# Optimization experiments

Hardware: AMD Instinct MI355X
Metric: run time of the kernel (lower is better)

The kernel has to match this reference:

```python
import jax, jax.numpy as jnp
import numpy as np

D_MODEL = 2048
D_INNER = 4096      # expand * d_model
HEADDIM = 64
NHEADS = 64         # d_inner // headdim
D_STATE = 128
NGROUPS = 1
D_CONV = 4
CHUNK = 128
EPS = 1e-5
BATCH = 2
SEQLEN = 4096
D_CONV_CH = D_INNER + 2 * NGROUPS * D_STATE            # 4352
D_IN_PROJ = 2 * D_INNER + 2 * NGROUPS * D_STATE + NHEADS  # 8512


def setup_inputs() -> dict:
    ks = jax.random.split(jax.random.key(0), 9)
    u = jax.random.normal(ks[0], (BATCH, SEQLEN, D_MODEL), jnp.float32)
    W_in = jax.random.normal(ks[1], (D_MODEL, D_IN_PROJ), jnp.float32) * 0.02
    conv_w = jax.random.normal(ks[2], (D_CONV_CH, D_CONV), jnp.float32) * 0.2
    conv_b = jax.random.normal(ks[3], (D_CONV_CH,), jnp.float32) * 0.02
    dt_bias = jax.random.normal(ks[4], (NHEADS,), jnp.float32) * 0.1
    A_log = jax.random.normal(ks[5], (NHEADS,), jnp.float32) * 0.1
    D = jnp.ones((NHEADS,), jnp.float32)
    norm_w = jnp.ones((D_INNER,), jnp.float32)
    W_out = jax.random.normal(ks[8], (D_INNER, D_MODEL), jnp.float32) * 0.02
    return dict(u=u, W_in=W_in, conv_w=conv_w, conv_b=conv_b, dt_bias=dt_bias,
                A_log=A_log, D=D, norm_w=norm_w, W_out=W_out)


def _mamba2_forward(u, W_in, conv_w, conv_b, dt_bias, A_log, D, norm_w, W_out):
    b, L, _ = u.shape
    zxbcdt = u @ W_in                                       # (b, L, 8512)
    z = zxbcdt[..., :D_INNER]
    xBC = zxbcdt[..., D_INNER:D_INNER + D_CONV_CH]
    dt = zxbcdt[..., D_INNER + D_CONV_CH:]                  # (b, L, h)

    # causal depthwise conv1d (padding = d_conv-1, truncated to L) + SiLU
    padded = jnp.pad(xBC, ((0, 0), (D_CONV - 1, 0), (0, 0)))
    xBC_conv = conv_b + sum(padded[:, k:k + L, :] * conv_w[:, k] for k in range(D_CONV))
    xBC_act = jax.nn.silu(xBC_conv)

    x = xBC_act[..., :D_INNER].reshape(b, L, NHEADS, HEADDIM)
    Bm = xBC_act[..., D_INNER:D_INNER + NGROUPS * D_STATE].reshape(b, L, NGROUPS, D_STATE)
    Cm = xBC_act[..., D_INNER + NGROUPS * D_STATE:].reshape(b, L, NGROUPS, D_STATE)
    rep = NHEADS // NGROUPS
    Bh = jnp.repeat(Bm, rep, axis=2)                        # (b, L, h, n)
    Ch = jnp.repeat(Cm, rep, axis=2)

    A = -jnp.exp(A_log)                                     # (h,), negative
    dtf = jax.nn.softplus(dt + dt_bias)                     # (b, L, h)

    # ---- chunked SSD (structured state-space duality) scan ----
    nc = L // CHUNK
    xc = x.reshape(b, nc, CHUNK, NHEADS, HEADDIM)
    Bc = Bh.reshape(b, nc, CHUNK, NHEADS, D_STATE)
    Cc = Ch.reshape(b, nc, CHUNK, NHEADS, D_STATE)
    dtc = dtf.reshape(b, nc, CHUNK, NHEADS)
    cum = jnp.cumsum(dtc * A, axis=2)                       # (b, nc, cs, h), decreasing

    # intra-chunk causal decay matrix L_ij = exp(cum_i - cum_j), i >= j
    idx = jnp.arange(CHUNK)
    mask = (idx[:, None] >= idx[None, :])[None, None, :, :, None]
    seg = cum[:, :, :, None, :] - cum[:, :, None, :, :]     # (b, nc, i, j, h)
    decay = jnp.exp(jnp.where(mask, seg, -jnp.inf))
    CB = jnp.einsum('bcihn,bcjhn->bcijh', Cc, Bc)
    Y_diag = jnp.einsum('bcijh,bcjh,bcjhp->bcihp', CB * decay, dtc, xc)

    # per-chunk final states: sum_j exp(cum_last - cum_j) * dt_j * B_j (x) x_j
    decay_last = jnp.exp(cum[:, :, -1:, :] - cum)           # (b, nc, cs, h)
    states = jnp.einsum('bclh,bclhn,bclhp->bchpn', decay_last * dtc, Bc, xc)

    # inter-chunk recurrence: carry_{c+1} = exp(sum dA_c) * carry_c + states_c
    Atot = jnp.exp(cum[:, :, -1, :])                        # (b, nc, h)
    def step(carry, inp):
        a, s = inp
        return a[..., None, None] * carry + s, carry
    init = jnp.zeros((b, NHEADS, HEADDIM, D_STATE), jnp.float32)
    _, prev = jax.lax.scan(step, init, (jnp.moveaxis(Atot, 1, 0), jnp.moveaxis(states, 1, 0)))
    prev = jnp.moveaxis(prev, 0, 1)                         # (b, nc, h, p, n) state entering each chunk

    Y_off = jnp.einsum('bclhn,bclh,bchpn->bclhp', Cc, jnp.exp(cum), prev)

    y = (Y_diag + Y_off).reshape(b, L, NHEADS, HEADDIM) + D[:, None] * x
    y = y.reshape(b, L, D_INNER)

    # gated RMSNorm: rmsnorm(y * silu(z)) * norm_w
    t = y * jax.nn.silu(z)
    t = t * jax.lax.rsqrt(jnp.mean(t * t, axis=-1, keepdims=True) + EPS) * norm_w
    return t @ W_out


def reference(u, W_in, conv_w, conv_b, dt_bias, A_log, D, norm_w, W_out):
    return _mamba2_forward(u, W_in, conv_w, conv_b, dt_bias, A_log, D, norm_w, W_out)
```

## Files before the change

### kernel.cpp

```cpp
#include <hip/hip_runtime.h>

#define BATCH 2
#define SEQLEN 4096
#define DM 2048
#define DIP 8512
#define DIPP 8576
#define DI 4096
#define DCC 4352
#define NH 64
#define HD 64
#define DSZ 128
#define CHK 128
#define NC 32
#define NBL (BATCH*SEQLEN)
#define LDP 136

typedef __attribute__((ext_vector_type(4))) float f32x4;
typedef __attribute__((ext_vector_type(8))) __bf16 bf16x8;
typedef __attribute__((ext_vector_type(8))) unsigned short us8;
typedef __attribute__((ext_vector_type(4))) unsigned short us4;

__device__ inline float bf2f(unsigned short u){ union{unsigned int i; float f;} v; v.i=((unsigned)u)<<16; return v.f; }
__device__ inline unsigned short f2bf(float f){ union{float f; unsigned int i;} v; v.f=f; unsigned r=(v.i + 0x7FFFu + ((v.i>>16)&1u))>>16; return (unsigned short)r; }

#define GLOAD_LDS16(gp, lp) __builtin_amdgcn_global_load_lds( \
    (const __attribute__((address_space(1))) void*)(gp), \
    (__attribute__((address_space(3))) void*)(lp), 16, 0, 0)

__global__ void beacon_kernel(float* __restrict__ out, float v)
{
    if (blockIdx.x == 0 && threadIdx.x == 0) out[0] = v;
}

__global__ void cast_bf16_kernel(const float* __restrict__ src, unsigned short* __restrict__ dst, size_t n)
{
    size_t stride = (size_t)gridDim.x * blockDim.x * 8;
    for (size_t i = ((size_t)blockIdx.x*blockDim.x + threadIdx.x)*8; i < n; i += stride) {
        float4 a = *(const float4*)&src[i];
        float4 b = *(const float4*)&src[i+4];
        us8 o;
        o[0]=f2bf(a.x); o[1]=f2bf(a.y); o[2]=f2bf(a.z); o[3]=f2bf(a.w);
        o[4]=f2bf(b.x); o[5]=f2bf(b.y); o[6]=f2bf(b.z); o[7]=f2bf(b.w);
        *(us8*)&dst[i] = o;
    }
}

__global__ __launch_bounds__(256) void transpose_cast_kernel(
    const float* __restrict__ in, unsigned short* __restrict__ out, int R, int C)
{
    __shared__ float tile[32][33];
    const int c0 = blockIdx.x*32, r0 = blockIdx.y*32;
    const int tx = threadIdx.x & 31, ty = threadIdx.x >> 5;
    #pragma unroll
    for (int i = 0; i < 4; i++) {
        const int r = r0 + ty + i*8;
        const int c = c0 + tx;
        tile[ty+i*8][tx] = (c < C) ? in[(size_t)r*C + c] : 0.f;
    }
    __syncthreads();
    #pragma unroll
    for (int i = 0; i < 4; i++) {
        const int cc = c0 + ty + i*8;
        const int rr = r0 + tx;
        out[(size_t)cc*R + rr] = f2bf(tile[tx][ty+i*8]);
    }
}

template<int EPI>
__global__ __launch_bounds__(512, 2) void gemm256(
    const unsigned short* __restrict__ A, const unsigned short* __restrict__ Bt,
    float* __restrict__ C, int K, int ldc, int Nmax,
    unsigned short* __restrict__ zbf, unsigned short* __restrict__ xbcbf,
    float* __restrict__ dtf, const float* __restrict__ dt_bias)
{
    __shared__ unsigned short L[65536];
    const int m0 = blockIdx.x * 256;
    const int n0 = blockIdx.y * 256;
    const int tid = threadIdx.x;
    const int lane = tid & 63;
    const int wid  = tid >> 6;
    const int wm = wid >> 2, wn = wid & 3;
    const int lr  = lane & 15;
    const int lkg = (lane >> 4) * 8;
    const int srow = (wid << 4) + (lane >> 3);
    const int scol = ((lane & 7) ^ (lane >> 3)) << 3;
    const int cs0 = lkg ^ ((lr & 7) << 3);
    const int cs1 = cs0 ^ 32;
    const int nt = K >> 6;

    f32x4 acc[8][4];
    #pragma unroll
    for (int i=0;i<8;i++)
        #pragma unroll
        for (int j=0;j<4;j++) acc[i][j] = f32x4{0.f,0.f,0.f,0.f};

    auto stA = [&](int buf, int t, int h) {
        const unsigned short* g = A + (size_t)(m0 + h*128 + srow)*K + t*64 + scol;
        GLOAD_LDS16(g,               &L[buf*32768 + h*8192 + wid*1024]);
        GLOAD_LDS16(g + (size_t)8*K, &L[buf*32768 + h*8192 + wid*1024 + 512]);
    };
    auto stB = [&](int buf, int t, int h) {
        const int rr = n0 + h*128 + srow;
        const int r0 = (rr     > Nmax) ? Nmax : rr;
        const int r1 = (rr + 8 > Nmax) ? Nmax : rr + 8;
        GLOAD_LDS16(Bt + (size_t)r0*K + t*64 + scol, &L[buf*32768 + 16384 + h*8192 + wid*1024]);
        GLOAD_LDS16(Bt + (size_t)r1*K + t*64 + scol, &L[buf*32768 + 16384 + h*8192 + wid*1024 + 512]);
    };

    bf16x8 bfr[4][2];
    auto rdA = [&](int buf, int mq, int s, int ks) {
        const int rl = mq*32 + s*16 + lr;
        return *(const bf16x8*)&L[buf*32768 + wm*8192 + rl*64 + (ks ? cs1 : cs0)];
    };
    auto rdB = [&](int buf, int nf, int ks) {
        const int rl = (wn & 1)*64 + nf*16 + lr;
        return *(const bf16x8*)&L[buf*32768 + 16384 + (wn >> 1)*8192 + rl*64 + (ks ? cs1 : cs0)];
    };

#define PH(BUF, MQ, LOADB, ...) do { \
    bf16x8 af[2][2]; \
    af[0][0]=rdA(BUF,MQ,0,0); af[0][1]=rdA(BUF,MQ,0,1); \
    af[1][0]=rdA(BUF,MQ,1,0); af[1][1]=rdA(BUF,MQ,1,1); \
    if (LOADB) { \
        _Pragma("unroll") \
        for (int nf=0;nf<4;nf++){ bfr[nf][0]=rdB(BUF,nf,0); bfr[nf][1]=rdB(BUF,nf,1);} } \
    __VA_ARGS__; \
    asm volatile("s_barrier" ::: "memory"); \
    __builtin_amdgcn_s_setprio(1); \
    _Pragma("unroll") \
    for (int s=0;s<2;s++) { \
        _Pragma("unroll") \
        for (int nf=0;nf<4;nf++) { \
            acc[MQ*2+s][nf] = __builtin_amdgcn_mfma_f32_16x16x32_bf16(af[s][0], bfr[nf][0], acc[MQ*2+s][nf], 0,0,0); \
            acc[MQ*2+s][nf] = __builtin_amdgcn_mfma_f32_16x16x32_bf16(af[s][1], bfr[nf][1], acc[MQ*2+s][nf], 0,0,0); } } \
    __builtin_amdgcn_s_setprio(0); \
    asm volatile("s_barrier" ::: "memory"); \
} while(0)

    stA(0, 0, 0); stA(0, 0, 1); stB(0, 0, 0); stB(0, 0, 1);
    stB(1, 1, 0); stB(1, 1, 1);
    asm volatile("s_waitcnt vmcnt(4)" ::: "memory");
    asm volatile("s_barrier" ::: "memory");

    #pragma unroll 1
    for (int t = 0; t < nt; t += 2) {
        const int tp2 = (t + 2 < nt) ? t + 2 : nt - 1;
        const int tp3 = (t + 3 < nt) ? t + 3 : nt - 1;
        PH(0, 0, true,  stA(1, t+1, 0));
        PH(0, 1, false, stA(1, t+1, 1); stB(0, tp2, 0));
        PH(0, 2, false, stB(0, tp2, 1));
        PH(0, 3, false, asm volatile("s_waitcnt vmcnt(4)" ::: "memory"));
        PH(1, 0, true,  stA(0, tp2, 0));
        PH(1, 1, false, stA(0, tp2, 1); stB(1, tp3, 0));
        PH(1, 2, false, stB(1, tp3, 1));
        PH(1, 3, false, asm volatile("s_waitcnt vmcnt(4)" ::: "memory"));
    }
#undef PH

    const int cr = (lane >> 4) * 4;
    const int cc = lane & 15;
    #pragma unroll
    for (int i=0;i<8;i++) {
        #pragma unroll
        for (int j=0;j<4;j++) {
            const int row = m0 + wm*128 + i*16 + cr;
            const int col = n0 + wn*64 + j*16 + cc;
            #pragma unroll
            for (int r=0;r<4;r++) {
                const float val = acc[i][j][r];
                const int rr = row + r;
                if (EPI == 0) {
                    C[(size_t)rr*ldc + col] = val;
                } else {
                    if (col < DI) {
                        zbf[(size_t)rr*DI + col] = f2bf(val);
                    } else if (col < DI + DCC) {
                        xbcbf[(size_t)rr*DCC + (col - DI)] = f2bf(val);
                    } else if (col < DI + DCC + NH) {
                        const int hh = col - (DI + DCC);
                        const float x = val + dt_bias[hh];
                        dtf[(size_t)rr*NH + hh] = (x > 20.f) ? x : log1pf(__expf(x));
                    }
                }
            }
        }
    }
}

__global__ __launch_bounds__(256) void conv_x_kernel(
    const unsigned short* __restrict__ xbc,
    const float* __restrict__ cw, const float* __restrict__ cb,
    unsigned short* __restrict__ xT)
{
    __shared__ float raw[67][68];
    __shared__ unsigned short ot[64][72];
    const int lt = blockIdx.x;
    const int h  = blockIdx.y;
    const int b  = lt >> 6;
    const int l0 = (lt & 63) * 64;
    const int t = threadIdx.x;

    for (int i = t; i < 536; i += 256) {
        const int li = i >> 3, cg = (i & 7) * 8;
        const int l = l0 - 3 + li;
        us8 v;
        #pragma unroll
        for (int e = 0; e < 8; e++) v[e] = 0;
        if (l >= 0) v = *(const us8*)&xbc[(size_t)(b*SEQLEN + l)*DCC + h*64 + cg];
        #pragma unroll
        for (int e = 0; e < 8; e++) raw[li][cg+e] = bf2f(v[e]);
    }
    __syncthreads();
    #pragma unroll
    for (int j = 0; j < 16; j++) {
        const int i = t + j*256;
        const int l = i >> 6, p = i & 63;
        const int ch = h*64 + p;
        float a = cb[ch];
        #pragma unroll
        for (int k = 0; k < 4; k++) a += raw[l + k][p] * cw[ch*4 + k];
        a = a / (1.f + __expf(-a));
        ot[l][p] = f2bf(a);
    }
    __syncthreads();
    for (int i = t; i < 512; i += 256) {
        const int p = i >> 3, lg = (i & 7) * 8;
        us8 o;
        #pragma unroll
        for (int e = 0; e < 8; e++) o[e] = ot[lg + e][p];
        *(us8*)&xT[(size_t)((b*NH + h)*HD + p)*SEQLEN + l0 + lg] = o;
    }
}

__global__ void conv_bc_kernel(const unsigned short* __restrict__ xbc,
                               const float* __restrict__ cw, const float* __restrict__ cb,
                               unsigned short* __restrict__ bcbf)
{
    const int idx = blockIdx.x*256 + threadIdx.x;
    if (idx >= NBL*32) return;
    const int g = idx & 31;
    const int row = idx >> 5;
    const int l = row & (SEQLEN-1);
    const int ch0 = DI + g*8;
    float a[8];
    #pragma unroll
    for (int e=0;e<8;e++) a[e] = cb[ch0+e];
    #pragma unroll
    for (int k = 0; k < 4; k++) {
        if (l + k >= 3) {
            us8 v = *(const us8*)&xbc[(size_t)(row + k - 3)*DCC + ch0];
            #pragma unroll
            for (int e=0;e<8;e++) a[e] += bf2f(v[e]) * cw[(ch0+e)*4 + k];
        }
    }
    us8 o;
    #pragma unroll
    for (int e=0;e<8;e++){ const float s = a[e]/(1.f+__expf(-a[e])); o[e]=f2bf(s); }
    *(us8*)&bcbf[(size_t)row*256 + g*8] = o;
}

__global__ void cum_kernel(const float* __restrict__ dtf, const float* __restrict__ A_log,
                           float* __restrict__ cum)
{
    const int idx = blockIdx.x*256 + threadIdx.x;
    const int h = idx & 63;
    const int bc = idx >> 6;
    const float A = -__expf(A_log[h]);
    float c = 0.f;
    const float* src = dtf + (size_t)bc*CHK*NH + h;
    float* dst = cum + (size_t)bc*CHK*NH + h;
    for (int i = 0; i < CHK; i++) { c += src[i*NH]*A; dst[i*NH] = c; }
}

__global__ __launch_bounds__(256) void ssm_passS(
    const unsigned short* __restrict__ bcbf,
    const unsigned short* __restrict__ xT,
    const float* __restrict__ cumg,
    const float* __restrict__ dtfg,
    unsigned short* __restrict__ states)
{
    __shared__ unsigned short BT[128*LDP];
    __shared__ unsigned short XW[64*LDP];
    __shared__ float cum_s[128], dtc_s[128], w_s[128];

    const int blk = blockIdx.x;
    const int h = blk & 63;
    const int bc = blk >> 6;
    const int r0 = bc * CHK;
    const int t = threadIdx.x;
    const int lane = t & 63;
    const int wid = t >> 6;

    if (t < 128) {
        cum_s[t] = cumg[(size_t)(r0+t)*NH + h];
        dtc_s[t] = dtfg[(size_t)(r0+t)*NH + h];
    }
    for (int i = t; i < 2048; i += 256) {
        const int l = i >> 4, cg = (i & 15)*8;
        us8 v = *(const us8*)(bcbf + (size_t)(r0+l)*256 + cg);
        #pragma unroll
        for (int e = 0; e < 8; e++) BT[(cg+e)*LDP + l] = v[e];
    }
    __syncthreads();
    if (t < 128) w_s[t] = __expf(cum_s[127] - cum_s[t]) * dtc_s[t];
    __syncthreads();
    {
        const int b = bc >> 5;
        const int li = (bc & 31) * CHK;
        const unsigned short* xb = xT + (size_t)((b*NH + h)*HD)*SEQLEN + li;
        for (int i = t; i < 1024; i += 256) {
            const int p = i >> 4, cg = (i & 15)*8;
            us8 v = *(const us8*)(xb + (size_t)p*SEQLEN + cg);
            #pragma unroll
            for (int e = 0; e < 8; e++) v[e] = f2bf(bf2f(v[e]) * w_s[cg+e]);
            *(us8*)&XW[p*LDP + cg] = v;
        }
    }
    __syncthreads();

    const int lr = lane & 15;
    const int lkg = (lane >> 4)*8;
    const int wr = wid >> 1, wc = wid & 1;

    f32x4 acc[2][4];
    #pragma unroll
    for (int i=0;i<2;i++)
        #pragma unroll
        for (int j=0;j<4;j++) acc[i][j] = f32x4{0.f,0.f,0.f,0.f};
    #pragma unroll
    for (int k = 0; k < 4; k++) {
        bf16x8 a[2], b[4];
        #pragma unroll
        for (int i=0;i<2;i++) a[i] = *(const bf16x8*)&XW[(wr*32 + i*16 + lr)*LDP + k*32 + lkg];
        #pragma unroll
        for (int j=0;j<4;j++) b[j] = *(const bf16x8*)&BT[(wc*64 + j*16 + lr)*LDP + k*32 + lkg];
        #pragma unroll
        for (int i=0;i<2;i++)
            #pragma unroll
            for (int j=0;j<4;j++)
                acc[i][j] = __builtin_amdgcn_mfma_f32_16x16x32_bf16(a[i], b[j], acc[i][j], 0,0,0);
    }
    unsigned short* sb = states + (size_t)blk * (HD*DSZ);
    const int cr = (lane >> 4)*4, cc = lane & 15;
    #pragma unroll
    for (int i=0;i<2;i++) {
        #pragma unroll
        for (int j=0;j<4;j++) {
            const int nn = wc*64 + j*16 + cc;
            #pragma unroll
            for (int r=0;r<4;r++) {
                const int pp = wr*32 + i*16 + cr + r;
                sb[pp*DSZ + nn] = f2bf(acc[i][j][r]);
            }
        }
    }
}

__global__ void scan_kernel(unsigned short* __restrict__ states, const float* __restrict__ cumg)
{
    const int idx = blockIdx.x*256 + threadIdx.x;
    const int n = idx & 127;
    const int p = (idx >> 7) & 63;
    const int h = (idx >> 13) & 63;
    const int b = idx >> 19;
    float carry = 0.f;
    for (int c = 0; c < NC; c++) {
        const size_t off = ((size_t)((b*NC + c)*NH + h))*(HD*DSZ) + p*DSZ + n;
        const float s = bf2f(states[off]);
        states[off] = f2bf(carry);
        const float atot = __expf(cumg[(size_t)((b*NC+c)*CHK + 127)*NH + h]);
        carry = atot*carry + s;
    }
}

__global__ __launch_bounds__(256) void ssm_passY(
    const unsigned short* __restrict__ bcbf,
    const unsigned short* __restrict__ xT,
    const unsigned short* __restrict__ statesg,
    const float* __restrict__ cumg,
    const float* __restrict__ dtfg,
    const float* __restrict__ Dg,
    unsigned short* __restrict__ y)
{
    __shared__ unsigned short P1[128*LDP];
    __shared__ unsigned short P2[128*LDP];
    __shared__ unsigned short XTs[64*LDP];
    __shared__ unsigned short PV[64*LDP];
    __shared__ float cum_s[128], dtc_s[128];

    const int blk = blockIdx.x;
    const int h = blk & 63;
    const int bc = blk >> 6;
    const int r0 = bc * CHK;
    const int t = threadIdx.x;
    const int lane = t & 63;
    const int wid = t >> 6;

    if (t < 128) {
        cum_s[t] = cumg[(size_t)(r0+t)*NH + h];
        dtc_s[t] = dtfg[(size_t)(r0+t)*NH + h];
    }
    for (int i = t; i < 2048; i += 256) {
        const int l = i >> 4, cg = (i & 15)*8;
        const unsigned short* src = bcbf + (size_t)(r0+l)*256 + cg;
        *(us8*)&P2[l*LDP + cg] = *(const us8*)src;
        *(us8*)&P1[l*LDP + cg] = *(const us8*)(src + 128);
    }
    {
        const int b = bc >> 5;
        const int li = (bc & 31) * CHK;
        const unsigned short* xb = xT + (size_t)((b*NH + h)*HD)*SEQLEN + li;
        const unsigned short* sb = statesg + (size_t)blk * (HD*DSZ);
        for (int i = t; i < 1024; i += 256) {
            const int p = i >> 4, cg = (i & 15)*8;
            *(us8*)&XTs[p*LDP + cg] = *(const us8*)(xb + (size_t)p*SEQLEN + cg);
            *(us8*)&PV[p*LDP + cg]  = *(const us8*)(sb + p*DSZ + cg);
        }
    }
    __syncthreads();

    const int lr = lane & 15;
    const int lkg = (lane >> 4)*8;
    const int wr = wid >> 1, wc = wid & 1;

    f32x4 acc1[4][4], acc2[4][2];
    #pragma unroll
    for (int i=0;i<4;i++) {
        #pragma unroll
        for (int j=0;j<4;j++) acc1[i][j] = f32x4{0.f,0.f,0.f,0.f};
        #pragma unroll
        for (int j=0;j<2;j++) acc2[i][j] = f32x4{0.f,0.f,0.f,0.f};
    }
    #pragma unroll
    for (int k = 0; k < 4; k++) {
        bf16x8 a[4], b[4], pv[2];
        #pragma unroll
        for (int i=0;i<4;i++) a[i] = *(const bf16x8*)&P1[(wr*64 + i*16 + lr)*LDP + k*32 + lkg];
        #pragma unroll
        for (int j=0;j<4;j++) b[j] = *(const bf16x8*)&P2[(wc*64 + j*16 + lr)*LDP + k*32 + lkg];
        #pragma unroll
        for (int j=0;j<2;j++) pv[j] = *(const bf16x8*)&PV[(wc*32 + j*16 + lr)*LDP + k*32 + lkg];
        #pragma unroll
        for (int i=0;i<4;i++) {
            #pragma unroll
            for (int j=0;j<4;j++)
                acc1[i][j] = __builtin_amdgcn_mfma_f32_16x16x32_bf16(a[i], b[j], acc1[i][j], 0,0,0);
            #pragma unroll
            for (int j=0;j<2;j++)
                acc2[i][j] = __builtin_amdgcn_mfma_f32_16x16x32_bf16(a[i], pv[j], acc2[i][j], 0,0,0);
        }
    }
    __syncthreads();
    const int cr = (lane >> 4)*4, cc = lane & 15;
    #pragma unroll
    for (int i=0;i<4;i++) {
        #pragma unroll
        for (int j=0;j<4;j++) {
            const int jj = wc*64 + j*16 + cc;
            #pragma unroll
            for (int r=0;r<4;r++) {
                const int ii = wr*64 + i*16 + cr + r;
                float v = 0.f;
                if (jj <= ii) v = acc1[i][j][r] * __expf(cum_s[ii] - cum_s[jj]) * dtc_s[jj];
                P1[ii*LDP + jj] = f2bf(v);
            }
        }
    }
    __syncthreads();
    #pragma unroll
    for (int i=0;i<4;i++) {
        #pragma unroll
        for (int r=0;r<4;r++) {
            const int ii = wr*64 + i*16 + cr + r;
            const float sc = __expf(cum_s[ii]);
            #pragma unroll
            for (int j=0;j<2;j++) acc2[i][j][r] *= sc;
        }
    }
    #pragma unroll
    for (int k = 0; k < 4; k++) {
        bf16x8 a[4], x2[2];
        #pragma unroll
        for (int i=0;i<4;i++) a[i] = *(const bf16x8*)&P1[(wr*64 + i*16 + lr)*LDP + k*32 + lkg];
        #pragma unroll
        for (int j=0;j<2;j++) x2[j] = *(const bf16x8*)&XTs[(wc*32 + j*16 + lr)*LDP + k*32 + lkg];
        #pragma unroll
        for (int i=0;i<4;i++)
            #pragma unroll
            for (int j=0;j<2;j++)
                acc2[i][j] = __builtin_amdgcn_mfma_f32_16x16x32_bf16(a[i], x2[j], acc2[i][j], 0,0,0);
    }
    const float Dv = Dg[h];
    #pragma unroll
    for (int i=0;i<4;i++) {
        #pragma unroll
        for (int j=0;j<2;j++) {
            const int pp = wc*32 + j*16 + cc;
            #pragma unroll
            for (int r=0;r<4;r++) {
                const int ii = wr*64 + i*16 + cr + r;
                const float xv = bf2f(XTs[pp*LDP + ii]);
                y[(size_t)(r0+ii)*DI + h*64 + pp] = f2bf(acc2[i][j][r] + Dv * xv);
            }
        }
    }
}

__global__ __launch_bounds__(256) void gate_rms_kernel(
    const unsigned short* __restrict__ y, const unsigned short* __restrict__ z,
    const float* __restrict__ nw, unsigned short* __restrict__ tbf)
{
    const int row = blockIdx.x;
    const int t = threadIdx.x;
    const int lane = t & 63, wid = t >> 6;
    float tv[16];
    float ss = 0.f;
    #pragma unroll
    for (int i = 0; i < 2; i++) {
        const int c = (i*256 + t)*8;
        const us8 yv = *(const us8*)&y[(size_t)row*DI + c];
        const us8 zv = *(const us8*)&z[(size_t)row*DI + c];
        #pragma unroll
        for (int e = 0; e < 8; e++) {
            const float fy = bf2f(yv[e]);
            const float fz = bf2f(zv[e]);
            const float v = fy * (fz / (1.f + __expf(-fz)));
            tv[i*8+e] = v;
            ss += v*v;
        }
    }
    #pragma unroll
    for (int o = 1; o < 64; o <<= 1) ss += __shfl_xor(ss, o, 64);
    __shared__ float red[4];
    if (lane == 0) red[wid] = ss;
    __syncthreads();
    const float rms = rsqrtf((red[0]+red[1]+red[2]+red[3]) * (1.f/DI) + 1e-5f);
    #pragma unroll
    for (int i = 0; i < 2; i++) {
        const int c = (i*256 + t)*8;
        us8 o;
        #pragma unroll
        for (int e = 0; e < 8; e += 4) {
            const float4 wv = *(const float4*)&nw[c + e];
            o[e+0]=f2bf(tv[i*8+e+0]*rms*wv.x);
            o[e+1]=f2bf(tv[i*8+e+1]*rms*wv.y);
            o[e+2]=f2bf(tv[i*8+e+2]*rms*wv.z);
            o[e+3]=f2bf(tv[i*8+e+3]*rms*wv.w);
        }
        *(us8*)&tbf[(size_t)row*DI + c] = o;
    }
}

extern "C" void kernel_launch(void* const* d_in, const int* in_sizes, int n_in,
                              void* d_out, int out_size, void* d_ws, size_t ws_size,
                              hipStream_t stream)
{
    const float* u       = (const float*)d_in[0];
    const float* W_in    = (const float*)d_in[1];
    const float* conv_w  = (const float*)d_in[2];
    const float* conv_b  = (const float*)d_in[3];
    const float* dt_bias = (const float*)d_in[4];
    const float* A_log   = (const float*)d_in[5];
    const float* Dp      = (const float*)d_in[6];
    const float* norm_w  = (const float*)d_in[7];
    const float* W_out   = (const float*)d_in[8];
    float* out = (float*)d_out;

    char* ws = (char*)d_ws;
    const size_t OFF_WINT = 33554432;
    const size_t OFF_R2   = 68681728;
    const size_t OFF_R3   = 139984896;
    const size_t OFF_SM   = 207093760;
    const size_t NEED     = OFF_SM + 2097152 + 2097152 + 4194304;
    if (ws_size < NEED) {
        beacon_kernel<<<1, 64, 0, stream>>>(out, 10000.f + (float)(ws_size >> 20));
        return;
    }

    unsigned short* u_bf   = (unsigned short*)(ws);
    unsigned short* winT   = (unsigned short*)(ws + OFF_WINT);
    unsigned short* xTb    = (unsigned short*)(ws);
    unsigned short* t_bf   = (unsigned short*)(ws);
    unsigned short* xbc_bf = (unsigned short*)(ws + OFF_R2);
    unsigned short* y_bf   = (unsigned short*)(ws + OFF_R2);
    unsigned short* states = (unsigned short*)(ws + OFF_R3);
    unsigned short* woutT  = (unsigned short*)(ws + OFF_R3);
    float*          dtf    = (float*)(ws + OFF_SM);
    float*          cum    = (float*)(ws + OFF_SM + 2097152);
    unsigned short* bc_bf  = (unsigned short*)(ws + OFF_SM + 4194304);
    unsigned short* z_bf   = (unsigned short*)d_out;

    cast_bf16_kernel<<<2048, 256, 0, stream>>>(u, u_bf, (size_t)NBL*DM);
    transpose_cast_kernel<<<dim3(DIPP/32, DM/32), 256, 0, stream>>>(W_in, winT, DM, DIP);
    gemm256<1><<<dim3(NBL/256, (DIPP+255)/256), 512, 0, stream>>>(
        u_bf, winT, nullptr, DM, 0, DIPP-1, z_bf, xbc_bf, dtf, dt_bias);
    conv_x_kernel<<<dim3(NBL/64, NH), 256, 0, stream>>>(xbc_bf, conv_w, conv_b, xTb);
    conv_bc_kernel<<<(NBL*32)/256, 256, 0, stream>>>(xbc_bf, conv_w, conv_b, bc_bf);
    cum_kernel<<<16, 256, 0, stream>>>(dtf, A_log, cum);
    ssm_passS<<<BATCH*NC*NH, 256, 0, stream>>>(bc_bf, xTb, cum, dtf, states);
    scan_kernel<<<4096, 256, 0, stream>>>(states, cum);
    ssm_passY<<<BATCH*NC*NH, 256, 0, stream>>>(bc_bf, xTb, states, cum, dtf, Dp, y_bf);
    gate_rms_kernel<<<NBL, 256, 0, stream>>>(y_bf, z_bf, norm_w, t_bf);
    transpose_cast_kernel<<<dim3(DM/32, DI/32), 256, 0, stream>>>(W_out, woutT, DI, DM);
    gemm256<0><<<dim3(NBL/256, DM/256), 512, 0, stream>>>(
        t_bf, woutT, out, DI, DM, DM-1, nullptr, nullptr, nullptr, nullptr);
}
```

Baseline: 958.2 us.

## Fuse BC conv into conv_x, read SSM operands directly from global, tweak GEMM bounds

Folds the B/C depthwise convolution into conv_x_kernel as four extra block rows, removing one kernel launch. ssm_passS and ssm_passY drop most of their shared-memory staging and feed MFMA fragments straight from global memory, which cuts LDS use and allows three blocks per CU, at the cost of uncoalesced, latency-exposed global loads inside the MFMA loop. The GEMM launch bounds change from two blocks per CU to one, which gives the compiler more registers but lowers occupancy, and an lgkmcnt wait is added before the barrier. cum_kernel now launches 64 blocks of 64 threads.

```diff
diff --git a/kernel.cpp b/kernel.cpp
--- a/kernel.cpp
+++ b/kernel.cpp
@@ -67,7 +67,7 @@
 }
 
 template<int EPI>
-__global__ __launch_bounds__(512, 2) void gemm256(
+__global__ __launch_bounds__(512, 1) void gemm256(
     const unsigned short* __restrict__ A, const unsigned short* __restrict__ Bt,
     float* __restrict__ C, int K, int ldc, int Nmax,
     unsigned short* __restrict__ zbf, unsigned short* __restrict__ xbcbf,
@@ -106,8 +106,6 @@
         GLOAD_LDS16(Bt + (size_t)r0*K + t*64 + scol, &L[buf*32768 + 16384 + h*8192 + wid*1024]);
         GLOAD_LDS16(Bt + (size_t)r1*K + t*64 + scol, &L[buf*32768 + 16384 + h*8192 + wid*1024 + 512]);
     };
-
-    bf16x8 bfr[4][2];
     auto rdA = [&](int buf, int mq, int s, int ks) {
         const int rl = mq*32 + s*16 + lr;
         return *(const bf16x8*)&L[buf*32768 + wm*8192 + rl*64 + (ks ? cs1 : cs0)];
@@ -117,6 +115,7 @@
         return *(const bf16x8*)&L[buf*32768 + 16384 + (wn >> 1)*8192 + rl*64 + (ks ? cs1 : cs0)];
     };
 
+    bf16x8 bfr[4][2];
 #define PH(BUF, MQ, LOADB, ...) do { \
     bf16x8 af[2][2]; \
     af[0][0]=rdA(BUF,MQ,0,0); af[0][1]=rdA(BUF,MQ,0,1); \
@@ -125,14 +124,15 @@
         _Pragma("unroll") \
         for (int nf=0;nf<4;nf++){ bfr[nf][0]=rdB(BUF,nf,0); bfr[nf][1]=rdB(BUF,nf,1);} } \
     __VA_ARGS__; \
+    if (LOADB) asm volatile("s_waitcnt lgkmcnt(8)" ::: "memory"); \
     asm volatile("s_barrier" ::: "memory"); \
     __builtin_amdgcn_s_setprio(1); \
     _Pragma("unroll") \
     for (int s=0;s<2;s++) { \
         _Pragma("unroll") \
         for (int nf=0;nf<4;nf++) { \
-            acc[MQ*2+s][nf] = __builtin_amdgcn_mfma_f32_16x16x32_bf16(af[s][0], bfr[nf][0], acc[MQ*2+s][nf], 0,0,0); \
-            acc[MQ*2+s][nf] = __builtin_amdgcn_mfma_f32_16x16x32_bf16(af[s][1], bfr[nf][1], acc[MQ*2+s][nf], 0,0,0); } } \
+            acc[(MQ)*2+s][nf] = __builtin_amdgcn_mfma_f32_16x16x32_bf16(af[s][0], bfr[nf][0], acc[(MQ)*2+s][nf], 0,0,0); \
+            acc[(MQ)*2+s][nf] = __builtin_amdgcn_mfma_f32_16x16x32_bf16(af[s][1], bfr[nf][1], acc[(MQ)*2+s][nf], 0,0,0); } } \
     __builtin_amdgcn_s_setprio(0); \
     asm volatile("s_barrier" ::: "memory"); \
 } while(0)
@@ -190,7 +190,8 @@
 __global__ __launch_bounds__(256) void conv_x_kernel(
     const unsigned short* __restrict__ xbc,
     const float* __restrict__ cw, const float* __restrict__ cb,
-    unsigned short* __restrict__ xT)
+    unsigned short* __restrict__ xT,
+    unsigned short* __restrict__ bcbf)
 {
     __shared__ float raw[67][68];
     __shared__ unsigned short ot[64][72];
@@ -200,6 +201,33 @@
     const int l0 = (lt & 63) * 64;
     const int t = threadIdx.x;
 
+    if (h >= 64) {
+        const int g4 = h - 64;
+        #pragma unroll
+        for (int j = 0; j < 2; j++) {
+            const int u = t + j*256;
+            const int l = u >> 3, pg = (u & 7)*8;
+            const int ch0 = DI + g4*64 + pg;
+            const int row = b*SEQLEN + l0 + l;
+            float a[8];
+            #pragma unroll
+            for (int e=0;e<8;e++) a[e] = cb[ch0+e];
+            #pragma unroll
+            for (int k = 0; k < 4; k++) {
+                if (l0 + l + k >= 3) {
+                    us8 v = *(const us8*)&xbc[(size_t)(row + k - 3)*DCC + ch0];
+                    #pragma unroll
+                    for (int e=0;e<8;e++) a[e] += bf2f(v[e]) * cw[(ch0+e)*4 + k];
+                }
+            }
+            us8 o;
+            #pragma unroll
+            for (int e=0;e<8;e++){ const float s = a[e]/(1.f+__expf(-a[e])); o[e]=f2bf(s); }
+            *(us8*)&bcbf[(size_t)row*256 + g4*64 + pg] = o;
+        }
+        return;
+    }
+
     for (int i = t; i < 536; i += 256) {
         const int li = i >> 3, cg = (i & 7) * 8;
         const int l = l0 - 3 + li;
@@ -232,37 +260,11 @@
     }
 }
 
-__global__ void conv_bc_kernel(const unsigned short* __restrict__ xbc,
-                               const float* __restrict__ cw, const float* __restrict__ cb,
-                               unsigned short* __restrict__ bcbf)
-{
-    const int idx = blockIdx.x*256 + threadIdx.x;
-    if (idx >= NBL*32) return;
-    const int g = idx & 31;
-    const int row = idx >> 5;
-    const int l = row & (SEQLEN-1);
-    const int ch0 = DI + g*8;
-    float a[8];
-    #pragma unroll
-    for (int e=0;e<8;e++) a[e] = cb[ch0+e];
-    #pragma unroll
-    for (int k = 0; k < 4; k++) {
-        if (l + k >= 3) {
-            us8 v = *(const us8*)&xbc[(size_t)(row + k - 3)*DCC + ch0];
-            #pragma unroll
-            for (int e=0;e<8;e++) a[e] += bf2f(v[e]) * cw[(ch0+e)*4 + k];
-        }
-    }
-    us8 o;
-    #pragma unroll
-    for (int e=0;e<8;e++){ const float s = a[e]/(1.f+__expf(-a[e])); o[e]=f2bf(s); }
-    *(us8*)&bcbf[(size_t)row*256 + g*8] = o;
-}
-
 __global__ void cum_kernel(const float* __restrict__ dtf, const float* __restrict__ A_log,
                            float* __restrict__ cum)
 {
-    const int idx = blockIdx.x*256 + threadIdx.x;
+    const int idx = blockIdx.x*blockDim.x + threadIdx.x;
+    if (idx >= BATCH*NC*NH) return;
     const int h = idx & 63;
     const int bc = idx >> 6;
     const float A = -__expf(A_log[h]);
@@ -272,7 +274,7 @@
     for (int i = 0; i < CHK; i++) { c += src[i*NH]*A; dst[i*NH] = c; }
 }
 
-__global__ __launch_bounds__(256) void ssm_passS(
+__global__ __launch_bounds__(256, 3) void ssm_passS(
     const unsigned short* __restrict__ bcbf,
     const unsigned short* __restrict__ xT,
     const float* __restrict__ cumg,
@@ -280,8 +282,7 @@
     unsigned short* __restrict__ states)
 {
     __shared__ unsigned short BT[128*LDP];
-    __shared__ unsigned short XW[64*LDP];
-    __shared__ float cum_s[128], dtc_s[128], w_s[128];
+    __shared__ float w_s[128];
 
     const int blk = blockIdx.x;
     const int h = blk & 63;
@@ -292,8 +293,10 @@
     const int wid = t >> 6;
 
     if (t < 128) {
-        cum_s[t] = cumg[(size_t)(r0+t)*NH + h];
-        dtc_s[t] = dtfg[(size_t)(r0+t)*NH + h];
+        const float cl = cumg[(size_t)(r0+127)*NH + h];
+        const float ci = cumg[(size_t)(r0+t)*NH + h];
+        const float dt = dtfg[(size_t)(r0+t)*NH + h];
+        w_s[t] = __expf(cl - ci) * dt;
     }
     for (int i = t; i < 2048; i += 256) {
         const int l = i >> 4, cg = (i & 15)*8;
@@ -302,25 +305,13 @@
         for (int e = 0; e < 8; e++) BT[(cg+e)*LDP + l] = v[e];
     }
     __syncthreads();
-    if (t < 128) w_s[t] = __expf(cum_s[127] - cum_s[t]) * dtc_s[t];
-    __syncthreads();
-    {
-        const int b = bc >> 5;
-        const int li = (bc & 31) * CHK;
-        const unsigned short* xb = xT + (size_t)((b*NH + h)*HD)*SEQLEN + li;
-        for (int i = t; i < 1024; i += 256) {
-            const int p = i >> 4, cg = (i & 15)*8;
-            us8 v = *(const us8*)(xb + (size_t)p*SEQLEN + cg);
-            #pragma unroll
-            for (int e = 0; e < 8; e++) v[e] = f2bf(bf2f(v[e]) * w_s[cg+e]);
-            *(us8*)&XW[p*LDP + cg] = v;
-        }
-    }
-    __syncthreads();
 
     const int lr = lane & 15;
     const int lkg = (lane >> 4)*8;
     const int wr = wid >> 1, wc = wid & 1;
+    const int b = bc >> 5;
+    const int li = (bc & 31) * CHK;
+    const unsigned short* xb = xT + (size_t)((b*NH + h)*HD)*SEQLEN + li;
 
     f32x4 acc[2][4];
     #pragma unroll
@@ -329,16 +320,22 @@
         for (int j=0;j<4;j++) acc[i][j] = f32x4{0.f,0.f,0.f,0.f};
     #pragma unroll
     for (int k = 0; k < 4; k++) {
-        bf16x8 a[2], b[4];
-        #pragma unroll
-        for (int i=0;i<2;i++) a[i] = *(const bf16x8*)&XW[(wr*32 + i*16 + lr)*LDP + k*32 + lkg];
-        #pragma unroll
-        for (int j=0;j<4;j++) b[j] = *(const bf16x8*)&BT[(wc*64 + j*16 + lr)*LDP + k*32 + lkg];
+        bf16x8 a[2], bfr[4];
+        #pragma unroll
+        for (int i=0;i<2;i++) {
+            us8 xv = *(const us8*)(xb + (size_t)(wr*32 + i*16 + lr)*SEQLEN + k*32 + lkg);
+            us8 aw;
+            #pragma unroll
+            for (int e=0;e<8;e++) aw[e] = f2bf(bf2f(xv[e]) * w_s[k*32 + lkg + e]);
+            a[i] = __builtin_bit_cast(bf16x8, aw);
+        }
+        #pragma unroll
+        for (int j=0;j<4;j++) bfr[j] = *(const bf16x8*)&BT[(wc*64 + j*16 + lr)*LDP + k*32 + lkg];
         #pragma unroll
         for (int i=0;i<2;i++)
             #pragma unroll
             for (int j=0;j<4;j++)
-                acc[i][j] = __builtin_amdgcn_mfma_f32_16x16x32_bf16(a[i], b[j], acc[i][j], 0,0,0);
+                acc[i][j] = __builtin_amdgcn_mfma_f32_16x16x32_bf16(a[i], bfr[j], acc[i][j], 0,0,0);
     }
     unsigned short* sb = states + (size_t)blk * (HD*DSZ);
     const int cr = (lane >> 4)*4, cc = lane & 15;
@@ -373,7 +370,7 @@
     }
 }
 
-__global__ __launch_bounds__(256) void ssm_passY(
+__global__ __launch_bounds__(256, 3) void ssm_passY(
     const unsigned short* __restrict__ bcbf,
     const unsigned short* __restrict__ xT,
     const unsigned short* __restrict__ statesg,
@@ -383,9 +380,6 @@
     unsigned short* __restrict__ y)
 {
     __shared__ unsigned short P1[128*LDP];
-    __shared__ unsigned short P2[128*LDP];
-    __shared__ unsigned short XTs[64*LDP];
-    __shared__ unsigned short PV[64*LDP];
     __shared__ float cum_s[128], dtc_s[128];
 
     const int blk = blockIdx.x;
@@ -402,26 +396,18 @@
     }
     for (int i = t; i < 2048; i += 256) {
         const int l = i >> 4, cg = (i & 15)*8;
-        const unsigned short* src = bcbf + (size_t)(r0+l)*256 + cg;
-        *(us8*)&P2[l*LDP + cg] = *(const us8*)src;
-        *(us8*)&P1[l*LDP + cg] = *(const us8*)(src + 128);
-    }
-    {
-        const int b = bc >> 5;
-        const int li = (bc & 31) * CHK;
-        const unsigned short* xb = xT + (size_t)((b*NH + h)*HD)*SEQLEN + li;
-        const unsigned short* sb = statesg + (size_t)blk * (HD*DSZ);
-        for (int i = t; i < 1024; i += 256) {
-            const int p = i >> 4, cg = (i & 15)*8;
-            *(us8*)&XTs[p*LDP + cg] = *(const us8*)(xb + (size_t)p*SEQLEN + cg);
-            *(us8*)&PV[p*LDP + cg]  = *(const us8*)(sb + p*DSZ + cg);
-        }
+        *(us8*)&P1[l*LDP + cg] = *(const us8*)(bcbf + (size_t)(r0+l)*256 + 128 + cg);
     }
     __syncthreads();
 
     const int lr = lane & 15;
     const int lkg = (lane >> 4)*8;
     const int wr = wid >> 1, wc = wid & 1;
+    const int b = bc >> 5;
+    const int li = (bc & 31) * CHK;
+    const unsigned short* xb = xT + (size_t)((b*NH + h)*HD)*SEQLEN + li;
+    const unsigned short* sb = statesg + (size_t)blk * (HD*DSZ);
+    const unsigned short* bb = bcbf + (size_t)r0*256;
 
     f32x4 acc1[4][4], acc2[4][2];
     #pragma unroll
@@ -433,18 +419,18 @@
     }
     #pragma unroll
     for (int k = 0; k < 4; k++) {
-        bf16x8 a[4], b[4], pv[2];
+        bf16x8 a[4], bfr[4], pv[2];
         #pragma unroll
         for (int i=0;i<4;i++) a[i] = *(const bf16x8*)&P1[(wr*64 + i*16 + lr)*LDP + k*32 + lkg];
         #pragma unroll
-        for (int j=0;j<4;j++) b[j] = *(const bf16x8*)&P2[(wc*64 + j*16 + lr)*LDP + k*32 + lkg];
-        #pragma unroll
-        for (int j=0;j<2;j++) pv[j] = *(const bf16x8*)&PV[(wc*32 + j*16 + lr)*LDP + k*32 + lkg];
+        for (int j=0;j<4;j++) bfr[j] = *(const bf16x8*)(bb + (size_t)(wc*64 + j*16 + lr)*256 + k*32 + lkg);
+        #pragma unroll
+        for (int j=0;j<2;j++) pv[j] = *(const bf16x8*)(sb + (size_t)(wc*32 + j*16 + lr)*DSZ + k*32 + lkg);
         #pragma unroll
         for (int i=0;i<4;i++) {
             #pragma unroll
             for (int j=0;j<4;j++)
-                acc1[i][j] = __builtin_amdgcn_mfma_f32_16x16x32_bf16(a[i], b[j], acc1[i][j], 0,0,0);
+                acc1[i][j] = __builtin_amdgcn_mfma_f32_16x16x32_bf16(a[i], bfr[j], acc1[i][j], 0,0,0);
             #pragma unroll
             for (int j=0;j<2;j++)
                 acc2[i][j] = __builtin_amdgcn_mfma_f32_16x16x32_bf16(a[i], pv[j], acc2[i][j], 0,0,0);
@@ -483,7 +469,7 @@
         #pragma unroll
         for (int i=0;i<4;i++) a[i] = *(const bf16x8*)&P1[(wr*64 + i*16 + lr)*LDP + k*32 + lkg];
         #pragma unroll
-        for (int j=0;j<2;j++) x2[j] = *(const bf16x8*)&XTs[(wc*32 + j*16 + lr)*LDP + k*32 + lkg];
+        for (int j=0;j<2;j++) x2[j] = *(const bf16x8*)(xb + (size_t)(wc*32 + j*16 + lr)*SEQLEN + k*32 + lkg);
         #pragma unroll
         for (int i=0;i<4;i++)
             #pragma unroll
@@ -499,7 +485,7 @@
             #pragma unroll
             for (int r=0;r<4;r++) {
                 const int ii = wr*64 + i*16 + cr + r;
-                const float xv = bf2f(XTs[pp*LDP + ii]);
+                const float xv = bf2f(xb[(size_t)pp*SEQLEN + ii]);
                 y[(size_t)(r0+ii)*DI + h*64 + pp] = f2bf(acc2[i][j][r] + Dv * xv);
             }
         }
@@ -594,9 +580,8 @@
     transpose_cast_kernel<<<dim3(DIPP/32, DM/32), 256, 0, stream>>>(W_in, winT, DM, DIP);
     gemm256<1><<<dim3(NBL/256, (DIPP+255)/256), 512, 0, stream>>>(
         u_bf, winT, nullptr, DM, 0, DIPP-1, z_bf, xbc_bf, dtf, dt_bias);
-    conv_x_kernel<<<dim3(NBL/64, NH), 256, 0, stream>>>(xbc_bf, conv_w, conv_b, xTb);
-    conv_bc_kernel<<<(NBL*32)/256, 256, 0, stream>>>(xbc_bf, conv_w, conv_b, bc_bf);
-    cum_kernel<<<16, 256, 0, stream>>>(dtf, A_log, cum);
+    conv_x_kernel<<<dim3(NBL/64, NH+4), 256, 0, stream>>>(xbc_bf, conv_w, conv_b, xTb, bc_bf);
+    cum_kernel<<<64, 64, 0, stream>>>(dtf, A_log, cum);
     ssm_passS<<<BATCH*NC*NH, 256, 0, stream>>>(bc_bf, xTb, cum, dtf, states);
     scan_kernel<<<4096, 256, 0, stream>>>(states, cum);
     ssm_passY<<<BATCH*NC*NH, 256, 0, stream>>>(bc_bf, xTb, states, cum, dtf, Dp, y_bf);
```

New measurement: 871.8 us. 9.0% less time.
